# Optimization experiments

Measured on AMD Instinct MI355X. Metric: run time of the kernel, lower is better.

The kernel has to match this reference:

```python
import jax, jax.numpy as jnp
import numpy as np

U = 100000          # unique pillars
N = 2 * U           # voxels (2 per pillar -> unq_cnt==2, mask all True)
NUM_BINS = 32       # z bins
C_IN = 5
C_HID = 32          # out_channels // 2 in conv1d MLP
C_OUT = 64
R = 4               # channel-attention reduction
K = 7               # bin-attention conv kernel


def setup_inputs() -> dict:
    key = jax.random.key(0)
    ks = jax.random.split(key, 12)
    voxel_features = jax.random.normal(ks[0], (N, C_IN), jnp.float32)
    # each pillar p owns voxels 2p, 2p+1 placed in two distinct bins -> no scatter collision
    bins = (jnp.arange(N, dtype=jnp.int32) % NUM_BINS)
    voxel_coords = jnp.zeros((N, 4), jnp.int32).at[:, 1].set(bins)
    unq_coords = jnp.arange(U, dtype=jnp.int32)
    unq_inv = jnp.arange(N, dtype=jnp.int32) // 2
    unq_cnt = jnp.full((U,), 2, jnp.int32)
    s = 0.3
    return {
        'voxel_features': voxel_features,
        'voxel_coords': voxel_coords,
        'unq_coords': unq_coords,
        'unq_inv': unq_inv,
        'unq_cnt': unq_cnt,
        # up_dimension MLP (Linear(5,32) -> relu -> Linear(32,64))
        'W1': jax.random.normal(ks[1], (C_IN, C_HID), jnp.float32) * s,
        'b1': jnp.zeros((C_HID,), jnp.float32),
        'W2': jax.random.normal(ks[2], (C_HID, C_OUT), jnp.float32) * s,
        'b2': jnp.zeros((C_OUT,), jnp.float32),
        # ZBAM channel-attention shared MLP
        'Wc1': jax.random.normal(ks[3], (C_OUT, C_OUT // R), jnp.float32) * s,
        'bc1': jnp.zeros((C_OUT // R,), jnp.float32),
        'Wc2': jax.random.normal(ks[4], (C_OUT // R, C_OUT), jnp.float32) * s,
        'bc2': jnp.zeros((C_OUT,), jnp.float32),
        # ZBAM bin (spatial) attention: conv1d over bins, 2->1 channels, kernel 7
        'Wsp': jax.random.normal(ks[5], (1, 2, K), jnp.float32) * s,
        'bsp': jnp.zeros((1,), jnp.float32),
    }


def _cbam_forward(voxel_features, W1, b1, W2, b2, Wc1, bc1, Wc2, bc2, Wsp, bsp,
                  voxel_coords, unq_coords, unq_inv, unq_cnt):
    n_pillars = unq_coords.shape[0]
    # --- binning: scatter voxels into (pillar, z-bin) slots ---
    src = jnp.zeros((n_pillars, NUM_BINS, voxel_features.shape[1]), voxel_features.dtype)
    src = src.at[unq_inv, voxel_coords[:, 1]].set(voxel_features)
    occupied_mask = unq_cnt >= 2  # all True by construction -> src[mask] == src
    # --- up_dimension MLP: (U, bins, 5) -> (U, bins, 64) ---
    x = jax.nn.relu(src @ W1 + b1) @ W2 + b2
    x = jnp.transpose(x, (0, 2, 1))  # (U, C, bins)
    # --- ZBAM channel attention ---
    avg_p = x.mean(axis=2)
    max_p = x.max(axis=2)
    mlp = lambda v: jax.nn.relu(v @ Wc1 + bc1) @ Wc2 + bc2
    att_c = jax.nn.sigmoid(mlp(avg_p) + mlp(max_p))  # (U, C)
    x = x * att_c[:, :, None]
    # --- ZBAM bin attention (conv over z-bins) ---
    s = jnp.stack([x.mean(axis=1), x.max(axis=1)], axis=1)  # (U, 2, bins)
    att_s = jax.lax.conv_general_dilated(
        s, Wsp, window_strides=(1,), padding=[(K // 2, K // 2)],
        dimension_numbers=('NCH', 'OIH', 'NCH')) + bsp  # (U, 1, bins)
    x = x * jax.nn.sigmoid(att_s)
    # --- max-pool over bins ---
    return x.max(axis=2), occupied_mask


def reference(voxel_features, voxel_coords, unq_coords, unq_inv, unq_cnt,
              W1, b1, W2, b2, Wc1, bc1, Wc2, bc2, Wsp, bsp):
    return _cbam_forward(voxel_features, W1, b1, W2, b2, Wc1, bc1, Wc2, bc2,
                         Wsp, bsp, voxel_coords, unq_coords, unq_inv, unq_cnt)
```

## Files before the change

### kernel.cpp

```cpp
#include <hip/hip_runtime.h>
#include <math.h>


#define CO 64

typedef __attribute__((ext_vector_type(8))) short s16x8;
typedef __attribute__((ext_vector_type(4))) float f32x4;
union ABu { uint4 u4; s16x8 s; };

__device__ __forceinline__ float sgm(float x) {
  return 1.0f / (1.0f + __expf(-x));
}
template <int PAT>
__device__ __forceinline__ float qadd(float s) {
  int t = __builtin_amdgcn_update_dpp(0, __builtin_bit_cast(int, s),
                                      PAT, 0xf, 0xf, true);
  return s + __builtin_bit_cast(float, t);
}
template <int PAT>
__device__ __forceinline__ float qmaxd(float m) {
  int t = __builtin_amdgcn_update_dpp(__builtin_bit_cast(int, m),
                                      __builtin_bit_cast(int, m),
                                      PAT, 0xf, 0xf, false);
  return fmaxf(m, __builtin_bit_cast(float, t));
}
template <int PAT>
__device__ __forceinline__ float qmind(float m) {
  int t = __builtin_amdgcn_update_dpp(__builtin_bit_cast(int, m),
                                      __builtin_bit_cast(int, m),
                                      PAT, 0xf, 0xf, false);
  return fminf(m, __builtin_bit_cast(float, t));
}
__device__ __forceinline__ float qsum4(float s) { return qadd<0x4E>(qadd<0xB1>(s)); }
__device__ __forceinline__ float qmax4(float m) { return qmaxd<0x4E>(qmaxd<0xB1>(m)); }
__device__ __forceinline__ float qmin4(float m) { return qmind<0x4E>(qmind<0xB1>(m)); }
__device__ __forceinline__ void drain_lds() {
  __builtin_amdgcn_wave_barrier();
  __builtin_amdgcn_s_waitcnt(0xC07F);
  __builtin_amdgcn_wave_barrier();
}
__device__ __forceinline__ void drain_vm() {
  __builtin_amdgcn_wave_barrier();
  __builtin_amdgcn_s_waitcnt(0x0F70);
  __builtin_amdgcn_wave_barrier();
}

__device__ __forceinline__ uint rtn16(float f) {
  uint u = __builtin_bit_cast(uint, f);
  return u + 0x7fffu + ((u >> 16) & 1u);
}
__device__ __forceinline__ uint cvtpk(float a, float b) {
  uint r;
  asm("v_cvt_pk_bf16_f32 %0, %1, %2" : "=v"(r) : "v"(a), "v"(b));
  return r;
}
__device__ __forceinline__ void mk_frag(const float* e, ABu& hi, ABu& lo) {
  uint h[4], l[4];
#pragma unroll
  for (int p = 0; p < 4; ++p) {
    h[p] = cvtpk(e[2 * p], e[2 * p + 1]);
    float d0 = e[2 * p]     - __builtin_bit_cast(float, h[p] << 16);
    float d1 = e[2 * p + 1] - __builtin_bit_cast(float, h[p] & 0xffff0000u);
    l[p] = cvtpk(d0, d1);
  }
  hi.u4 = make_uint4(h[0], h[1], h[2], h[3]);
  lo.u4 = make_uint4(l[0], l[1], l[2], l[3]);
}

__global__ __launch_bounds__(256) void pack_kernel(
    const float* __restrict__ vf, const int* __restrict__ vcoord,
    const int* __restrict__ unq_inv, float* __restrict__ pvox, int n) {
  int i = blockIdx.x * blockDim.x + threadIdx.x;
  if (i >= n) return;
  int p = unq_inv[i];
  int slot = (i > 0 && unq_inv[i - 1] == p) ? 1 : 0;
  float* dst = pvox + 8 * (size_t)(2 * p + slot);
#pragma unroll
  for (int k = 0; k < 5; ++k) dst[k] = vf[5 * i + k];
  ((int*)dst)[5] = vcoord[4 * i + 1];
}

__global__ __launch_bounds__(256) void cbam_kernel(
    const float* __restrict__ pvox, const int* __restrict__ unq_cnt,
    const float* __restrict__ W1, const float* __restrict__ b1,
    const float* __restrict__ W2, const float* __restrict__ b2,
    const float* __restrict__ Wc1, const float* __restrict__ bc1,
    const float* __restrict__ Wc2, const float* __restrict__ bc2,
    const float* __restrict__ Wsp, const float* __restrict__ bsp,
    float* __restrict__ out, int U, int ngroups, int totalWaves) {
  __shared__ __align__(16) uint4 w2fh[256], w2fl[256];
  __shared__ __align__(16) float w1b[160], b1b[32];
  __shared__ __align__(16) float wc1b[1024];
  __shared__ __align__(16) float wc2b[1024];
  __shared__ __align__(16) float c0b[64], b2b[64], bc2b[64], bc1b[16];
  __shared__ __align__(16) float wsmx[64];
  __shared__ __align__(16) float wtab[16];
  __shared__ __align__(16) float vbuf[4][256];
  __shared__ __align__(16) float4 ybuf[4][144];

  const int tid = threadIdx.x;

  {
    const int nt = tid >> 6, l = tid & 63, gg = l >> 4, cc = l & 15;
    uint hu[4], lu[4];
#pragma unroll
    for (int p = 0; p < 4; ++p) {
      float f0 = W2[(8 * gg + 2 * p)     * 64 + 16 * nt + cc];
      float f1 = W2[(8 * gg + 2 * p + 1) * 64 + 16 * nt + cc];
      uint r0 = rtn16(f0), r1 = rtn16(f1);
      hu[p] = (r0 >> 16) | (r1 & 0xffff0000u);
      float d0 = f0 - __builtin_bit_cast(float, r0 & 0xffff0000u);
      float d1 = f1 - __builtin_bit_cast(float, r1 & 0xffff0000u);
      uint s0 = rtn16(d0), s1 = rtn16(d1);
      lu[p] = (s0 >> 16) | (s1 & 0xffff0000u);
    }
    w2fh[tid] = make_uint4(hu[0], hu[1], hu[2], hu[3]);
    w2fl[tid] = make_uint4(lu[0], lu[1], lu[2], lu[3]);
  }
  if (tid < 160) w1b[tid] = W1[tid];
  if (tid < 32) b1b[tid] = b1[tid];
  for (int i = tid; i < 1024; i += 256) {
    int ch = i >> 4, j = i & 15, qq = ch >> 4, k = ch & 15;
    wc1b[(4 * k + qq) * 16 + j] = Wc1[i];
    wc2b[(4 * k + qq) * 16 + j] = Wc2[j * 64 + ch];
  }
  if (tid < 64) { b2b[tid] = b2[tid]; bc2b[tid] = bc2[tid]; }
  if (tid < 16) bc1b[tid] = bc1[tid];
  if (tid < 32) {
    float sm = 0.0f, sx = 0.0f;
    for (int k = 0; k < 7; ++k)
      if ((unsigned)(tid + k - 3) < 32u) { sm += Wsp[k]; sx += Wsp[7 + k]; }
    wsmx[2 * tid] = sm; wsmx[2 * tid + 1] = sx;
  }
  if (tid < 8) {
    float a = 0.0f, b = 0.0f;
    if (tid < 7) { a = Wsp[tid]; b = Wsp[7 + tid]; }
    wtab[2 * tid] = a; wtab[2 * tid + 1] = b;
  }
  __syncthreads();
  if (tid < 64) {
    float c = b2b[tid];
    for (int j = 0; j < 32; ++j) c += fmaxf(b1b[j], 0.0f) * W2[j * 64 + tid];
    c0b[tid] = c;
  }
  __syncthreads();

  const int wv = tid >> 6, lane = tid & 63;
  int grp = blockIdx.x * 4 + wv;
  if (grp >= ngroups) return;

  float* const vb = vbuf[wv];
  float4* const vb4 = (float4*)vb;
  float4* const yb4 = ybuf[wv];
  float2* const yb2 = (float2*)yb4;

  const int c16 = lane & 15, g = lane >> 4;
  const int q = lane & 3, pp = lane >> 2;
  const float4* pv4 = (const float4*)pvox;
  const int f4max = 4 * U - 1;

  {
    int idx = 64 * grp + lane;
    idx = idx < f4max ? idx : f4max;
    __builtin_amdgcn_global_load_lds(
        (const __attribute__((address_space(1))) void*)(pv4 + idx),
        (__attribute__((address_space(3))) void*)vb4, 16, 0, 0);
  }
  drain_vm();

  for (; grp < ngroups; grp += totalWaves) {
    int ofs0 = 0;
    asm volatile("" : "+s"(ofs0));

    const int P0 = grp * 16;

    const int pg = P0 + pp;
    const int pc = pg < U ? pg : (U - 1);
    const int cnt = unq_cnt[pc];
    const int* vbi = (const int*)vb;
    const int b0 = vbi[(2 * pp) * 8 + 5] & 31;
    const int b1raw = vbi[(2 * pp + 1) * 8 + 5];

    ABu ah0, al0, ah1, al1;
    {
      const float4* vb4c = (const float4*)vb;
      float4 xa = vb4c[2 * c16], xb = vb4c[2 * c16 + 1];
      float4 yc = vb4c[2 * (c16 + 16)], yd = vb4c[2 * (c16 + 16) + 1];
      float va[5] = {xa.x, xa.y, xa.z, xa.w, xb.x};
      float vc[5] = {yc.x, yc.y, yc.z, yc.w, yd.x};
      const float4* w1b4 = (const float4*)w1b;
      const float4* b1b4 = (const float4*)b1b;
      float4 bA = b1b4[ofs0 + 2 * g], bB = b1b4[ofs0 + 2 * g + 1];
      float e0[8] = {bA.x, bA.y, bA.z, bA.w, bB.x, bB.y, bB.z, bB.w};
      float e1[8] = {bA.x, bA.y, bA.z, bA.w, bB.x, bB.y, bB.z, bB.w};
#pragma unroll
      for (int d = 0; d < 5; ++d) {
        float4 w0 = w1b4[ofs0 + d * 8 + 2 * g];
        float4 w1v = w1b4[ofs0 + d * 8 + 2 * g + 1];
        e0[0] += va[d] * w0.x;  e0[1] += va[d] * w0.y;
        e0[2] += va[d] * w0.z;  e0[3] += va[d] * w0.w;
        e0[4] += va[d] * w1v.x; e0[5] += va[d] * w1v.y;
        e0[6] += va[d] * w1v.z; e0[7] += va[d] * w1v.w;
        e1[0] += vc[d] * w0.x;  e1[1] += vc[d] * w0.y;
        e1[2] += vc[d] * w0.z;  e1[3] += vc[d] * w0.w;
        e1[4] += vc[d] * w1v.x; e1[5] += vc[d] * w1v.y;
        e1[6] += vc[d] * w1v.z; e1[7] += vc[d] * w1v.w;
      }
#pragma unroll
      for (int i = 0; i < 8; ++i) {
        e0[i] = fmaxf(e0[i], 0.0f);
        e1[i] = fmaxf(e1[i], 0.0f);
      }
      mk_frag(e0, ah0, al0);
      mk_frag(e1, ah1, al1);
    }
    drain_lds();

    {
      const int nxt = grp + totalWaves;
      if (nxt < ngroups) {
        int nidx = 64 * nxt + lane;
        nidx = nidx < f4max ? nidx : f4max;
        __builtin_amdgcn_global_load_lds(
            (const __attribute__((address_space(1))) void*)(pv4 + nidx),
            (__attribute__((address_space(3))) void*)vb4, 16, 0, 0);
      }
    }

    float y0[16], y1[16];
#pragma unroll
    for (int nt = 0; nt < 4; ++nt) {
      ABu bh, bl;
      bh.u4 = w2fh[ofs0 + nt * 64 + lane];
      bl.u4 = w2fl[ofs0 + nt * 64 + lane];
      f32x4 acc[2];
      acc[0] = 0; acc[1] = 0;
      acc[0] = __builtin_amdgcn_mfma_f32_16x16x32_bf16(ah0.s, bh.s, acc[0], 0, 0, 0);
      acc[0] = __builtin_amdgcn_mfma_f32_16x16x32_bf16(al0.s, bh.s, acc[0], 0, 0, 0);
      acc[0] = __builtin_amdgcn_mfma_f32_16x16x32_bf16(ah0.s, bl.s, acc[0], 0, 0, 0);
      acc[0] = __builtin_amdgcn_mfma_f32_16x16x32_bf16(al0.s, bl.s, acc[0], 0, 0, 0);
      acc[1] = __builtin_amdgcn_mfma_f32_16x16x32_bf16(ah1.s, bh.s, acc[1], 0, 0, 0);
      acc[1] = __builtin_amdgcn_mfma_f32_16x16x32_bf16(al1.s, bh.s, acc[1], 0, 0, 0);
      acc[1] = __builtin_amdgcn_mfma_f32_16x16x32_bf16(ah1.s, bl.s, acc[1], 0, 0, 0);
      acc[1] = __builtin_amdgcn_mfma_f32_16x16x32_bf16(al1.s, bl.s, acc[1], 0, 0, 0);
      const float b2v = b2b[16 * nt + c16];
#pragma unroll
      for (int mt = 0; mt < 2; ++mt)
#pragma unroll
        for (int rp = 0; rp < 2; ++rp) {
          const int p = 8 * mt + 2 * g + rp;
          float2 v2;
          v2.x = acc[mt][2 * rp]     + b2v;
          v2.y = acc[mt][2 * rp + 1] + b2v;
          yb2[p * 18 + c16] = v2;
        }
      if (q == nt) {
#pragma unroll
        for (int kk = 0; kk < 8; ++kk) {
          float4 t = yb4[pp * 9 + kk];
          y0[2 * kk]     = t.x; y1[2 * kk]     = t.y;
          y0[2 * kk + 1] = t.z; y1[2 * kk + 1] = t.w;
        }
      }
    }

    const bool has2 = (cnt >= 2);
    const int b1e = has2 ? (b1raw & 31) : 64;
#pragma unroll
    for (int k = 0; k < 16; ++k) y1[k] = has2 ? y1[k] : y0[k];

    float gq[16];
    const float kf = has2 ? 30.0f : 31.0f;
    const float inv32 = 1.0f / 32.0f;
    const float4* c04 = (const float4*)c0b;
    const float4* wc14 = (const float4*)wc1b;
    const float4* bc14 = (const float4*)bc1b;
#pragma unroll
    for (int jp = 0; jp < 2; ++jp) {
      float ha[8] = {0}, hm[8] = {0};
#pragma unroll
      for (int kb = 0; kb < 4; ++kb) {
        float4 cq = c04[q * 4 + kb];
        float c0a[4] = {cq.x, cq.y, cq.z, cq.w};
#pragma unroll
        for (int i = 0; i < 4; ++i) {
          const int k = 4 * kb + i;
          const float c0v = c0a[i];
          const float sumy = y0[k] + (has2 ? y1[k] : 0.0f);
          const float avg = fmaf(c0v, kf, sumy) * inv32;
          const float mxv = fmaxf(fmaxf(y0[k], y1[k]), c0v);
#pragma unroll
          for (int jbl = 0; jbl < 2; ++jbl) {
            float4 w = wc14[(4 * k + q) * 4 + 2 * jp + jbl];
            ha[4 * jbl]     += avg * w.x; ha[4 * jbl + 1] += avg * w.y;
            ha[4 * jbl + 2] += avg * w.z; ha[4 * jbl + 3] += avg * w.w;
            hm[4 * jbl]     += mxv * w.x; hm[4 * jbl + 1] += mxv * w.y;
            hm[4 * jbl + 2] += mxv * w.z; hm[4 * jbl + 3] += mxv * w.w;
          }
        }
      }
#pragma unroll
      for (int jbl = 0; jbl < 2; ++jbl) {
        float4 bb = bc14[2 * jp + jbl];
        float bba[4] = {bb.x, bb.y, bb.z, bb.w};
#pragma unroll
        for (int i = 0; i < 4; ++i) {
          const float sa = qsum4(ha[4 * jbl + i]) + bba[i];
          const float sm = qsum4(hm[4 * jbl + i]) + bba[i];
          gq[8 * jp + 4 * jbl + i] = fmaxf(sa, 0.0f) + fmaxf(sm, 0.0f);
        }
      }
    }

    float attc[16];
    float sc = 0.0f, mc = -3.0e38f;
    float sy0 = 0.0f, my0 = -3.0e38f, sy1 = 0.0f, my1 = -3.0e38f;
    const float4* wc24 = (const float4*)wc2b;
    const float4* bc24 = (const float4*)bc2b;
#pragma unroll
    for (int kb = 0; kb < 4; ++kb) {
      float4 cq = c04[q * 4 + kb];
      float4 bq = bc24[q * 4 + kb];
      float c0a[4] = {cq.x, cq.y, cq.z, cq.w};
      float b2a[4] = {bq.x, bq.y, bq.z, bq.w};
#pragma unroll
      for (int i = 0; i < 4; ++i) {
        const int k = 4 * kb + i;
        float pre = 2.0f * b2a[i];
#pragma unroll
        for (int jb = 0; jb < 4; ++jb) {
          float4 w = wc24[(4 * k + q) * 4 + jb];
          pre += gq[4 * jb] * w.x + gq[4 * jb + 1] * w.y +
                 gq[4 * jb + 2] * w.z + gq[4 * jb + 3] * w.w;
        }
        const float a = sgm(pre);
        attc[k] = a;
        const float pc0 = a * c0a[i], py0 = a * y0[k], py1 = a * y1[k];
        sc += pc0;  mc = fmaxf(mc, pc0);
        sy0 += py0; my0 = fmaxf(my0, py0);
        sy1 += py1; my1 = fmaxf(my1, py1);
      }
    }
    sc = qsum4(sc);   mc = qmax4(mc);
    sy0 = qsum4(sy0); my0 = qmax4(my0);
    sy1 = qsum4(sy1); my1 = qmax4(my1);

    const float inv64 = 1.0f / 64.0f;
    const float Mn = sc * inv64, Mx = mc;
    const float dm0 = (sy0 - sc) * inv64, dx0 = my0 - mc;
    const float dm1 = (sy1 - sc) * inv64, dx1 = my1 - mc;
    const float bspr = bsp[0];
    const float2* ws2 = (const float2*)wsmx;
    const float2* wt2 = (const float2*)wtab;
    float maxE = -3.0e38f, minE = 3.0e38f, sv0 = -3.0e38f, sv1 = -3.0e38f;
#pragma unroll
    for (int k = 0; k < 8; ++k) {
      const int b = 8 * q + k;
      float2 ws = ws2[b];
      float acc2 = bspr + Mn * ws.x + Mx * ws.y;
      int k0 = b0 - b + 3;  k0 = ((unsigned)k0 <= 6u) ? k0 : 7;
      int k1 = b1e - b + 3; k1 = ((unsigned)k1 <= 6u) ? k1 : 7;
      float2 w0 = wt2[k0];
      float2 w1v = wt2[k1];
      acc2 += dm0 * w0.x + dx0 * w0.y + dm1 * w1v.x + dx1 * w1v.y;
      const bool o0 = (b == b0), o1 = (b == b1e);
      const bool oc = o0 || o1;
      maxE = fmaxf(maxE, oc ? -3.0e38f : acc2);
      minE = fminf(minE, oc ?  3.0e38f : acc2);
      sv0 = o0 ? acc2 : sv0;
      sv1 = o1 ? acc2 : sv1;
    }
    maxE = qmax4(maxE); minE = qmin4(minE);
    sv0 = qmax4(sv0);   sv1 = qmax4(sv1);
    const float sig0 = sgm(sv0);
    const float sig1 = has2 ? sgm(sv1) : sig0;
    const float sE = sgm(maxE), sI = sgm(minE);

    if (pg < U) {
      float4* ov = (float4*)(out + (size_t)pg * CO + 16 * q);
#pragma unroll
      for (int kb = 0; kb < 4; ++kb) {
        float4 cq = c04[q * 4 + kb];
        float c0a[4] = {cq.x, cq.y, cq.z, cq.w};
        float rr[4];
#pragma unroll
        for (int i = 0; i < 4; ++i) {
          const int k = 4 * kb + i;
          const float c0v = c0a[i];
          const float sel = (c0v >= 0.0f) ? sE : sI;
          const float m = fmaxf(fmaxf(y0[k] * sig0, y1[k] * sig1), c0v * sel);
          rr[i] = attc[k] * m;
        }
        float4 r; r.x = rr[0]; r.y = rr[1]; r.z = rr[2]; r.w = rr[3];
        ov[kb] = r;
      }
      if (q == 0) out[(size_t)U * CO + pg] = has2 ? 1.0f : 0.0f;
    }

    drain_vm();
  }
}

extern "C" void kernel_launch(void* const* d_in, const int* in_sizes, int n_in,
                              void* d_out, int out_size, void* d_ws, size_t ws_size,
                              hipStream_t stream) {
  const float* vf      = (const float*)d_in[0];
  const int*   vcoord  = (const int*)d_in[1];
  const int*   unq_inv = (const int*)d_in[3];
  const int*   unq_cnt = (const int*)d_in[4];
  const float* W1  = (const float*)d_in[5];
  const float* b1  = (const float*)d_in[6];
  const float* W2  = (const float*)d_in[7];
  const float* b2  = (const float*)d_in[8];
  const float* Wc1 = (const float*)d_in[9];
  const float* bc1 = (const float*)d_in[10];
  const float* Wc2 = (const float*)d_in[11];
  const float* bc2 = (const float*)d_in[12];
  const float* Wsp = (const float*)d_in[13];
  const float* bsp = (const float*)d_in[14];

  const int N = in_sizes[3];
  const int U = in_sizes[4];

  float* pvox = (float*)d_ws;

  pack_kernel<<<(N + 255) / 256, 256, 0, stream>>>(vf, vcoord, unq_inv, pvox, N);

  static int blocksPerCU = 0;
  if (blocksPerCU == 0) {
    hipFuncAttributes a{};
    blocksPerCU = 4;
    if (hipFuncGetAttributes(&a, (const void*)cbam_kernel) == hipSuccess) {
      int v8 = (a.numRegs > 0) ? ((a.numRegs + 7) & ~7) : 128;
      int byV = 512 / v8;
      int byL = (a.sharedSizeBytes > 0)
                    ? (int)(163840 / (int)a.sharedSizeBytes) : 4;
      int m = byV < byL ? byV : byL;
      if (m < 1) m = 1;
      if (m > 8) m = 8;
      blocksPerCU = m;
    }
  }

  const int ngroups = (U + 15) / 16;
  int blocks = 256 * blocksPerCU;
  const int maxBlocks = (ngroups + 3) / 4;
  if (blocks > maxBlocks) blocks = maxBlocks;
  const int totalWaves = blocks * 4;
  cbam_kernel<<<blocks, 256, 0, stream>>>(
      pvox, unq_cnt, W1, b1, W2, b2, Wc1, bc1, Wc2, bc2, Wsp, bsp,
      (float*)d_out, U, ngroups, totalWaves);
}
```

Baseline: 138.7 us.

## Run channel-attention first MLP layer on MFMA with split-bf16 weights

Replaces the scalar FMA loop for the first channel-attention MLP layer (64->16, avg and max paths) with bf16 MFMA 16x16x32 instructions. Wc1 is stored in shared memory as hi/lo bf16 pairs to keep near-fp32 accuracy, and inputs are staged through an enlarged per-wave scratch buffer to form fragments. The blocks-per-CU heuristic is also changed to step-wise register thresholds. The cost is extra LDS round trips, fragment conversion and four MFMAs per k-step, plus more shared memory, which may reduce occupancy.

```diff
diff --git a/kernel.cpp b/kernel.cpp
--- a/kernel.cpp
+++ b/kernel.cpp
@@ -89,14 +89,14 @@
     const float* __restrict__ Wsp, const float* __restrict__ bsp,
     float* __restrict__ out, int U, int ngroups, int totalWaves) {
   __shared__ __align__(16) uint4 w2fh[256], w2fl[256];
+  __shared__ __align__(16) uint4 wc1fh[128], wc1fl[128];
   __shared__ __align__(16) float w1b[160], b1b[32];
-  __shared__ __align__(16) float wc1b[1024];
   __shared__ __align__(16) float wc2b[1024];
   __shared__ __align__(16) float c0b[64], b2b[64], bc2b[64], bc1b[16];
   __shared__ __align__(16) float wsmx[64];
   __shared__ __align__(16) float wtab[16];
   __shared__ __align__(16) float vbuf[4][256];
-  __shared__ __align__(16) float4 ybuf[4][144];
+  __shared__ __align__(16) float ybuf[4][1088];
 
   const int tid = threadIdx.x;
 
@@ -117,11 +117,27 @@
     w2fh[tid] = make_uint4(hu[0], hu[1], hu[2], hu[3]);
     w2fl[tid] = make_uint4(lu[0], lu[1], lu[2], lu[3]);
   }
+  if (tid < 128) {
+    const int ks = tid >> 6, l = tid & 63, gg = l >> 4, cc = l & 15;
+    uint hu[4], lu[4];
+#pragma unroll
+    for (int p = 0; p < 4; ++p) {
+      float f0 = Wc1[(32 * ks + 8 * gg + 2 * p)     * 16 + cc];
+      float f1 = Wc1[(32 * ks + 8 * gg + 2 * p + 1) * 16 + cc];
+      uint r0 = rtn16(f0), r1 = rtn16(f1);
+      hu[p] = (r0 >> 16) | (r1 & 0xffff0000u);
+      float d0 = f0 - __builtin_bit_cast(float, r0 & 0xffff0000u);
+      float d1 = f1 - __builtin_bit_cast(float, r1 & 0xffff0000u);
+      uint s0 = rtn16(d0), s1 = rtn16(d1);
+      lu[p] = (s0 >> 16) | (s1 & 0xffff0000u);
+    }
+    wc1fh[tid] = make_uint4(hu[0], hu[1], hu[2], hu[3]);
+    wc1fl[tid] = make_uint4(lu[0], lu[1], lu[2], lu[3]);
+  }
   if (tid < 160) w1b[tid] = W1[tid];
   if (tid < 32) b1b[tid] = b1[tid];
   for (int i = tid; i < 1024; i += 256) {
     int ch = i >> 4, j = i & 15, qq = ch >> 4, k = ch & 15;
-    wc1b[(4 * k + qq) * 16 + j] = Wc1[i];
     wc2b[(4 * k + qq) * 16 + j] = Wc2[j * 64 + ch];
   }
   if (tid < 64) { b2b[tid] = b2[tid]; bc2b[tid] = bc2[tid]; }
@@ -151,8 +167,9 @@
 
   float* const vb = vbuf[wv];
   float4* const vb4 = (float4*)vb;
-  float4* const yb4 = ybuf[wv];
-  float2* const yb2 = (float2*)yb4;
+  float* const scr = ybuf[wv];
+  float4* const yb4 = (float4*)scr;
+  float2* const yb2 = (float2*)scr;
 
   const int c16 = lane & 15, g = lane >> 4;
   const int q = lane & 3, pp = lane >> 2;
@@ -270,48 +287,84 @@
     for (int k = 0; k < 16; ++k) y1[k] = has2 ? y1[k] : y0[k];
 
     float gq[16];
-    const float kf = has2 ? 30.0f : 31.0f;
-    const float inv32 = 1.0f / 32.0f;
-    const float4* c04 = (const float4*)c0b;
-    const float4* wc14 = (const float4*)wc1b;
-    const float4* bc14 = (const float4*)bc1b;
-#pragma unroll
-    for (int jp = 0; jp < 2; ++jp) {
-      float ha[8] = {0}, hm[8] = {0};
+    {
+      const float kf = has2 ? 30.0f : 31.0f;
+      const float inv32 = 1.0f / 32.0f;
+      const float4* c04 = (const float4*)c0b;
 #pragma unroll
       for (int kb = 0; kb < 4; ++kb) {
         float4 cq = c04[q * 4 + kb];
-        float c0a[4] = {cq.x, cq.y, cq.z, cq.w};
-#pragma unroll
-        for (int i = 0; i < 4; ++i) {
-          const int k = 4 * kb + i;
-          const float c0v = c0a[i];
-          const float sumy = y0[k] + (has2 ? y1[k] : 0.0f);
-          const float avg = fmaf(c0v, kf, sumy) * inv32;
-          const float mxv = fmaxf(fmaxf(y0[k], y1[k]), c0v);
-#pragma unroll
-          for (int jbl = 0; jbl < 2; ++jbl) {
-            float4 w = wc14[(4 * k + q) * 4 + 2 * jp + jbl];
-            ha[4 * jbl]     += avg * w.x; ha[4 * jbl + 1] += avg * w.y;
-            ha[4 * jbl + 2] += avg * w.z; ha[4 * jbl + 3] += avg * w.w;
-            hm[4 * jbl]     += mxv * w.x; hm[4 * jbl + 1] += mxv * w.y;
-            hm[4 * jbl + 2] += mxv * w.z; hm[4 * jbl + 3] += mxv * w.w;
-          }
-        }
-      }
-#pragma unroll
-      for (int jbl = 0; jbl < 2; ++jbl) {
-        float4 bb = bc14[2 * jp + jbl];
-        float bba[4] = {bb.x, bb.y, bb.z, bb.w};
-#pragma unroll
-        for (int i = 0; i < 4; ++i) {
-          const float sa = qsum4(ha[4 * jbl + i]) + bba[i];
-          const float sm = qsum4(hm[4 * jbl + i]) + bba[i];
-          gq[8 * jp + 4 * jbl + i] = fmaxf(sa, 0.0f) + fmaxf(sm, 0.0f);
-        }
-      }
-    }
-
+        float4 t;
+        t.x = fmaf(cq.x, kf, y0[4 * kb + 0] + (has2 ? y1[4 * kb + 0] : 0.0f)) * inv32;
+        t.y = fmaf(cq.y, kf, y0[4 * kb + 1] + (has2 ? y1[4 * kb + 1] : 0.0f)) * inv32;
+        t.z = fmaf(cq.z, kf, y0[4 * kb + 2] + (has2 ? y1[4 * kb + 2] : 0.0f)) * inv32;
+        t.w = fmaf(cq.w, kf, y0[4 * kb + 3] + (has2 ? y1[4 * kb + 3] : 0.0f)) * inv32;
+        *((float4*)(scr + pp * 68 + 16 * q) + kb) = t;
+      }
+      ABu ah[2], al[2];
+#pragma unroll
+      for (int ks = 0; ks < 2; ++ks) {
+        const float4* s4 = (const float4*)(scr + c16 * 68 + 32 * ks + 8 * g);
+        float4 p0 = s4[0], p1 = s4[1];
+        float e[8] = {p0.x, p0.y, p0.z, p0.w, p1.x, p1.y, p1.z, p1.w};
+        mk_frag(e, ah[ks], al[ks]);
+      }
+      f32x4 accA = 0;
+#pragma unroll
+      for (int ks = 0; ks < 2; ++ks) {
+        ABu bh, bl;
+        bh.u4 = wc1fh[ofs0 + ks * 64 + lane];
+        bl.u4 = wc1fl[ofs0 + ks * 64 + lane];
+        accA = __builtin_amdgcn_mfma_f32_16x16x32_bf16(ah[ks].s, bh.s, accA, 0, 0, 0);
+        accA = __builtin_amdgcn_mfma_f32_16x16x32_bf16(al[ks].s, bh.s, accA, 0, 0, 0);
+        accA = __builtin_amdgcn_mfma_f32_16x16x32_bf16(ah[ks].s, bl.s, accA, 0, 0, 0);
+        accA = __builtin_amdgcn_mfma_f32_16x16x32_bf16(al[ks].s, bl.s, accA, 0, 0, 0);
+      }
+#pragma unroll
+      for (int kb = 0; kb < 4; ++kb) {
+        float4 cq = c04[q * 4 + kb];
+        float4 t;
+        t.x = fmaxf(fmaxf(y0[4 * kb + 0], y1[4 * kb + 0]), cq.x);
+        t.y = fmaxf(fmaxf(y0[4 * kb + 1], y1[4 * kb + 1]), cq.y);
+        t.z = fmaxf(fmaxf(y0[4 * kb + 2], y1[4 * kb + 2]), cq.z);
+        t.w = fmaxf(fmaxf(y0[4 * kb + 3], y1[4 * kb + 3]), cq.w);
+        *((float4*)(scr + pp * 68 + 16 * q) + kb) = t;
+      }
+#pragma unroll
+      for (int ks = 0; ks < 2; ++ks) {
+        const float4* s4 = (const float4*)(scr + c16 * 68 + 32 * ks + 8 * g);
+        float4 p0 = s4[0], p1 = s4[1];
+        float e[8] = {p0.x, p0.y, p0.z, p0.w, p1.x, p1.y, p1.z, p1.w};
+        mk_frag(e, ah[ks], al[ks]);
+      }
+      f32x4 accM = 0;
+#pragma unroll
+      for (int ks = 0; ks < 2; ++ks) {
+        ABu bh, bl;
+        bh.u4 = wc1fh[ofs0 + ks * 64 + lane];
+        bl.u4 = wc1fl[ofs0 + ks * 64 + lane];
+        accM = __builtin_amdgcn_mfma_f32_16x16x32_bf16(ah[ks].s, bh.s, accM, 0, 0, 0);
+        accM = __builtin_amdgcn_mfma_f32_16x16x32_bf16(al[ks].s, bh.s, accM, 0, 0, 0);
+        accM = __builtin_amdgcn_mfma_f32_16x16x32_bf16(ah[ks].s, bl.s, accM, 0, 0, 0);
+        accM = __builtin_amdgcn_mfma_f32_16x16x32_bf16(al[ks].s, bl.s, accM, 0, 0, 0);
+      }
+      const float bc1v = bc1b[c16];
+#pragma unroll
+      for (int r = 0; r < 4; ++r) {
+        const float gv = fmaxf(accA[r] + bc1v, 0.0f) +
+                         fmaxf(accM[r] + bc1v, 0.0f);
+        scr[(4 * g + r) * 20 + c16] = gv;
+      }
+      const float4* g4 = (const float4*)(scr + pp * 20);
+#pragma unroll
+      for (int jb = 0; jb < 4; ++jb) {
+        float4 t = g4[jb];
+        gq[4 * jb] = t.x; gq[4 * jb + 1] = t.y;
+        gq[4 * jb + 2] = t.z; gq[4 * jb + 3] = t.w;
+      }
+    }
+
+    const float4* c04 = (const float4*)c0b;
     float attc[16];
     float sc = 0.0f, mc = -3.0e38f;
     float sy0 = 0.0f, my0 = -3.0e38f, sy1 = 0.0f, my1 = -3.0e38f;
@@ -431,8 +484,12 @@
     hipFuncAttributes a{};
     blocksPerCU = 4;
     if (hipFuncGetAttributes(&a, (const void*)cbam_kernel) == hipSuccess) {
-      int v8 = (a.numRegs > 0) ? ((a.numRegs + 7) & ~7) : 128;
-      int byV = 512 / v8;
+      int byV = 4;
+      if (a.numRegs > 0) {
+        if (a.numRegs <= 64) byV = 8;
+        else if (a.numRegs <= 128) byV = 4;
+        else byV = 2;
+      }
       int byL = (a.sharedSizeBytes > 0)
                     ? (int)(163840 / (int)a.sharedSizeBytes) : 4;
       int m = byV < byL ? byV : byL;
```

New measurement: 130.7 us. -5.8%, faster.
